# Kernel tuning notes

Measured on AMD Instinct MI355X. Metric: run time of the kernel, lower is better.

The kernel has to match this reference:

```python
import jax, jax.numpy as jnp
import numpy as np
from jax import lax

DIM = 384
NUM_HEADS = 8
KV_NUM_HEADS = 2
REP = NUM_HEADS // KV_NUM_HEADS  # 4
KV_DIM = DIM * 2 // REP          # 192
EPS_LN = 1e-5
EPS_NORM = 1e-12


def _layernorm_channel(x, w, b):
    # WithBias LayerNorm over channel dim of NCHW tensor (matches to_3d -> LN(c) -> to_4d)
    mu = jnp.mean(x, axis=1, keepdims=True)
    var = jnp.var(x, axis=1, keepdims=True)
    return (x - mu) / jnp.sqrt(var + EPS_LN) * w[None, :, None, None] + b[None, :, None, None]


def _conv1x1(x, w):
    # w: [out, in] ; x: [b, in, h, w]
    return jnp.einsum('oi,bihw->bohw', w, x)


def _dwconv3x3(x, w):
    # depthwise 3x3, padding=1; w: [C, 1, 3, 3]
    C = x.shape[1]
    return lax.conv_general_dilated(
        x, w, window_strides=(1, 1), padding=((1, 1), (1, 1)),
        feature_group_count=C,
        dimension_numbers=('NCHW', 'OIHW', 'NCHW'))


def _l2norm(x):
    n = jnp.linalg.norm(x, axis=-1, keepdims=True)
    return x / jnp.maximum(n, EPS_NORM)


def setup_inputs() -> dict:
    key = jax.random.key(0)
    ks = jax.random.split(key, 8)
    b, h, w = 8, 128, 128
    scale1 = 1.0 / np.sqrt(DIM)
    return {
        'q': jax.random.normal(ks[0], (b, DIM, h, w), dtype=jnp.float32),
        'k': jax.random.normal(ks[1], (b, DIM, h, w), dtype=jnp.float32),
        'w_q': jax.random.normal(ks[2], (DIM, DIM), dtype=jnp.float32) * scale1,
        'w_kv': jax.random.normal(ks[3], (KV_DIM, DIM), dtype=jnp.float32) * scale1,
        'w_q_dw': jax.random.normal(ks[4], (DIM, 1, 3, 3), dtype=jnp.float32) * (1.0 / 3.0),
        'w_kv_dw': jax.random.normal(ks[5], (KV_DIM, 1, 3, 3), dtype=jnp.float32) * (1.0 / 3.0),
        'w_out': jax.random.normal(ks[6], (DIM, DIM), dtype=jnp.float32) * scale1,
        'temperature': jnp.ones((NUM_HEADS, 1, 1), dtype=jnp.float32),
        'lnq_w': jnp.ones((DIM,), dtype=jnp.float32),
        'lnq_b': jnp.zeros((DIM,), dtype=jnp.float32),
        'lnk_w': jnp.ones((DIM,), dtype=jnp.float32),
        'lnk_b': jnp.zeros((DIM,), dtype=jnp.float32),
    }


def reference(q, k, w_q, w_kv, w_q_dw, w_kv_dw, w_out, temperature,
              lnq_w, lnq_b, lnk_w, lnk_b):
    b, c, h, w = q.shape
    hw = h * w
    qn = _layernorm_channel(q, lnq_w, lnq_b)
    kn = _layernorm_channel(k, lnk_w, lnk_b)
    qp = _dwconv3x3(_conv1x1(qn, w_q), w_q_dw)          # [b, dim, h, w]
    kv = _dwconv3x3(_conv1x1(kn, w_kv), w_kv_dw)        # [b, 2*dim/rep, h, w]
    kk, vv = jnp.split(kv, 2, axis=1)                   # each [b, dim/rep, h, w]
    # reshape to heads: channel-attention layout [b, head, c_head, hw]
    qh = qp.reshape(b, NUM_HEADS, DIM // NUM_HEADS, hw)
    kh = kk.reshape(b, KV_NUM_HEADS, DIM // NUM_HEADS, hw)
    vh = vv.reshape(b, KV_NUM_HEADS, DIM // NUM_HEADS, hw)
    # GQA repeat kv heads (repeat_interleave on head dim)
    kh = jnp.repeat(kh, REP, axis=1)
    vh = jnp.repeat(vh, REP, axis=1)
    qh = _l2norm(qh)
    kh = _l2norm(kh)
    attn = jnp.einsum('bhck,bhdk->bhcd', qh, kh) * temperature[None]
    attn = jax.nn.softmax(attn, axis=-1)
    out = jnp.einsum('bhcd,bhdk->bhck', attn, vh)       # [b, head, c_head, hw]
    out = out.reshape(b, DIM, h, w)
    return _conv1x1(out, w_out)
```

## Files before the change

kernel.cpp:

```cpp
#include <hip/hip_runtime.h>
#include <math.h>


typedef unsigned short u16;
typedef unsigned int u32;
typedef short s16x8 __attribute__((ext_vector_type(8)));
typedef float f32x4 __attribute__((ext_vector_type(4)));

#define HW 16384
#define NB 8
#define CDIM 384
#define KVC 192

__device__ __forceinline__ float b2f(u16 u) {
  return __uint_as_float(((u32)u) << 16);
}
__device__ __forceinline__ u16 f2b(float f) {
  u32 u = __float_as_uint(f);
  u += 0x7fffu + ((u >> 16) & 1u);
  return (u16)(u >> 16);
}
__device__ __forceinline__ u32 pack2(float a, float c) {
  return (u32)f2b(a) | ((u32)f2b(c) << 16);
}

__global__ void k0_prep(const float* __restrict__ wq, const float* __restrict__ wkv,
                        const float* __restrict__ wo,
                        const float* __restrict__ lnqw, const float* __restrict__ lnqb,
                        const float* __restrict__ lnkw, const float* __restrict__ lnkb,
                        u16* __restrict__ wqp, float* __restrict__ rwsQ, float* __restrict__ biasQ,
                        u16* __restrict__ wkvp, float* __restrict__ rwsKV, float* __restrict__ biasKV,
                        u16* __restrict__ wop) {
  int r = blockIdx.x * 256 + threadIdx.x;
  if (r < 384) {
    float rs = 0.f, bs = 0.f;
    for (int i = 0; i < 384; ++i) {
      float wp = wq[r * 384 + i] * lnqw[i];
      u16 h = f2b(wp);
      rs += b2f(h);
      bs += wq[r * 384 + i] * lnqb[i];
      wqp[r * 384 + i] = h;
    }
    rwsQ[r] = rs; biasQ[r] = bs;
  } else if (r < 768) {
    int o = r - 384;
    if (o < 192) {
      float rs = 0.f, bs = 0.f;
      for (int i = 0; i < 384; ++i) {
        float wp = wkv[o * 384 + i] * lnkw[i];
        u16 h = f2b(wp);
        rs += b2f(h);
        bs += wkv[o * 384 + i] * lnkb[i];
        wkvp[o * 384 + i] = h;
      }
      rwsKV[o] = rs; biasKV[o] = bs;
    } else {
      for (int i = 0; i < 384; ++i) wkvp[o * 384 + i] = 0;
      rwsKV[o] = 0.f; biasKV[o] = 0.f;
    }
  } else if (r < 1152) {
    int o = r - 768;
    for (int i = 0; i < 384; ++i) wop[o * 384 + i] = f2b(wo[o * 384 + i]);
  }
}

__global__ __launch_bounds__(512, 4) void gemm_qkv(const u16* __restrict__ Aq,
                                                   const u16* __restrict__ Akv,
                                                   const float* __restrict__ qsrc,
                                                   const float* __restrict__ ksrc,
                                                   const float* __restrict__ rwsQ,
                                                   const float* __restrict__ biasQ,
                                                   const float* __restrict__ rwsKV,
                                                   const float* __restrict__ biasKV,
                                                   u16* __restrict__ qp, u16* __restrict__ kvp) {
  __shared__ __align__(16) char smem[53760];
  u16*    tB   = (u16*)smem;
  float2* sred = (float2*)(smem + 49152);
  float*  muL  = (float*)(smem + 53248);
  float*  sdL  = (float*)(smem + 53504);
  u16*    chB16 = (u16*)smem;

  const int zz = blockIdx.z;
  const bool isQ = (zz < 8);
  const int b = zz & 7;
  const u16* A = isQ ? Aq : Akv;
  const float* Bf = isQ ? qsrc : ksrc;
  const float* rowsum = isQ ? rwsQ : rwsKV;
  const float* bias = isQ ? biasQ : biasKV;
  u16* outp = isQ ? qp : kvp;
  const int M = isQ ? 384 : 192;

  const int pt = ((blockIdx.x & 7) << 5) | (blockIdx.x >> 3);
  const int tid = threadIdx.x;
  const int w = tid >> 6, l = tid & 63;
  const int lr = l & 15, lg = l >> 4;

  f32x4 acc[3][4] = {};

  {
    const size_t fbase = (size_t)b * CDIM * HW + (size_t)pt * 64 + l;
    float v[48];
#pragma unroll
    for (int it = 0; it < 12; ++it)
#pragma unroll
      for (int j = 0; j < 4; ++j)
        v[it * 4 + j] = Bf[fbase + (size_t)(it * 32 + w * 4 + j) * HW];

    float s_ = 0.f, q_ = 0.f;
#pragma unroll
    for (int it = 0; it < 12; ++it) {
      float v0 = v[it * 4], v1 = v[it * 4 + 1], v2 = v[it * 4 + 2], v3 = v[it * 4 + 3];
      s_ += (v0 + v1) + (v2 + v3);
      q_ += (v0 * v0 + v1 * v1) + (v2 * v2 + v3 * v3);
      u32 lo = pack2(v0, v1), hi = pack2(v2, v3);
      int cidx = it * 4 + (w >> 1);
      int off = l * 384 + ((cidx ^ (l & 7)) << 3) + (w & 1) * 4;
      *(uint2*)&tB[off] = make_uint2(lo, hi);
    }
    sred[w * 64 + l] = make_float2(s_, q_);
  }
  __syncthreads();

  if (tid < 64) {
    float s = 0.f, q2 = 0.f;
#pragma unroll
    for (int g = 0; g < 8; ++g) { float2 t = sred[g * 64 + tid]; s += t.x; q2 += t.y; }
    float mn = s * (1.f / 384.f);
    float var = q2 * (1.f / 384.f) - mn * mn;
    muL[tid] = mn;
    sdL[tid] = rsqrtf(var + 1e-5f);
  }
  __syncthreads();

  s16x8 a[2][3], bb[2][4];
#pragma unroll
  for (int mf = 0; mf < 3; ++mf)
    a[0][mf] = *(const s16x8*)(A + (size_t)(w * 48 + mf * 16 + lr) * 384 + lg * 8);
#pragma unroll
  for (int nf = 0; nf < 4; ++nf) {
    int row = nf * 16 + lr;
    bb[0][nf] = *(const s16x8*)&tB[row * 384 + ((lg ^ (row & 7)) << 3)];
  }
#pragma unroll
  for (int ks = 0; ks < 12; ++ks) {
    const int cur = ks & 1, nxt = cur ^ 1;
    if (ks < 11) {
      const int ko = (ks + 1) * 32 + lg * 8;
      const int cidx = (ks + 1) * 4 + lg;
#pragma unroll
      for (int mf = 0; mf < 3; ++mf)
        a[nxt][mf] = *(const s16x8*)(A + (size_t)(w * 48 + mf * 16 + lr) * 384 + ko);
#pragma unroll
      for (int nf = 0; nf < 4; ++nf) {
        int row = nf * 16 + lr;
        bb[nxt][nf] = *(const s16x8*)&tB[row * 384 + ((cidx ^ (row & 7)) << 3)];
      }
    }
#pragma unroll
    for (int mf = 0; mf < 3; ++mf)
#pragma unroll
      for (int nf = 0; nf < 4; ++nf)
        acc[mf][nf] = __builtin_amdgcn_mfma_f32_16x16x32_bf16(a[cur][mf], bb[cur][nf], acc[mf][nf], 0, 0, 0);
  }

#pragma unroll
  for (int cc = 0; cc < 2; ++cc) {
    __syncthreads();
    if ((w >> 2) == cc) {
#pragma unroll
      for (int nf = 0; nf < 4; ++nf) {
        int prow = nf * 16 + lr;
        float m_ = muL[prow], s_ = sdL[prow];
#pragma unroll
        for (int mf = 0; mf < 3; ++mf)
#pragma unroll
          for (int r = 0; r < 4; ++r) {
            int orow = w * 48 + mf * 16 + lg * 4 + r;
            float v = s_ * (acc[mf][nf][r] - m_ * rowsum[orow]) + bias[orow];
            chB16[((w & 3) * 48 + mf * 16 + lg * 4 + r) * 72 + prow] = f2b(v);
          }
      }
    }
    __syncthreads();
    for (int i = tid; i < 192 * 8; i += 512) {
      int row = i >> 3, c8 = i & 7;
      int g = cc * 192 + row;
      if (g < M) {
        uint4 v = *(const uint4*)&chB16[row * 72 + c8 * 8];
        *(uint4*)(outp + ((size_t)(b * M + g)) * HW + pt * 64 + c8 * 8) = v;
      }
    }
  }
}

__global__ __launch_bounds__(256) void k4_dw(const u16* __restrict__ qp, const u16* __restrict__ kvp,
                                             const float* __restrict__ wqdw, const float* __restrict__ wkvdw,
                                             u16* __restrict__ qd, u16* __restrict__ kvd,
                                             float* __restrict__ rnq, float* __restrict__ rnk) {
  __shared__ u16 plane[16384];
  __shared__ float red[256];

  int c = blockIdx.x, b = blockIdx.y;
  int tid = threadIdx.x;
  const u16* in; u16* outb; const float* wp; int C;
  int isQ = (c < 384), cc = isQ ? c : c - 384;
  if (isQ) { in = qp; outb = qd; wp = wqdw + cc * 9; C = CDIM; }
  else     { in = kvp; outb = kvd; wp = wkvdw + cc * 9; C = KVC; }
  size_t base = ((size_t)(b * C + cc)) * HW;

  float w[9];
#pragma unroll
  for (int j = 0; j < 9; ++j) w[j] = wp[j];

  const uint4* gsrc = (const uint4*)(in + base);
  uint4* lplane = (uint4*)plane;
#pragma unroll
  for (int i = 0; i < 8; ++i) lplane[tid + i * 256] = gsrc[tid + i * 256];
  __syncthreads();

  uint4* gdst = (uint4*)(outb + base);
  float ns = 0.f;
#pragma unroll
  for (int it = 0; it < 8; ++it) {
    int idx = tid + it * 256;
    int y = idx >> 4, ox = idx & 15;
    int x0 = ox * 8;

    float r[3][10];
#pragma unroll
    for (int rr = 0; rr < 3; ++rr) {
      int yy = y + rr - 1;
      if ((unsigned)yy < 128u) {
        int rbase = yy * 128 + x0;
        r[rr][0] = (x0 > 0) ? b2f(plane[rbase - 1]) : 0.f;
        uint4 v = *(const uint4*)&plane[rbase];
        u32 ws[4] = {v.x, v.y, v.z, v.w};
#pragma unroll
        for (int j = 0; j < 4; ++j) {
          r[rr][1 + 2 * j] = b2f((u16)(ws[j] & 0xffff));
          r[rr][2 + 2 * j] = b2f((u16)(ws[j] >> 16));
        }
        r[rr][9] = (x0 < 120) ? b2f(plane[rbase + 8]) : 0.f;
      } else {
#pragma unroll
        for (int j = 0; j < 10; ++j) r[rr][j] = 0.f;
      }
    }

    u32 packed[4];
#pragma unroll
    for (int j = 0; j < 8; ++j) {
      float a = 0.f;
#pragma unroll
      for (int rr = 0; rr < 3; ++rr)
#pragma unroll
        for (int dx = 0; dx < 3; ++dx)
          a += w[rr * 3 + dx] * r[rr][j + dx];
      u16 h = f2b(a);
      float hv = b2f(h);
      ns += hv * hv;
      if (j & 1) packed[j >> 1] |= ((u32)h) << 16; else packed[j >> 1] = (u32)h;
    }
    gdst[idx] = make_uint4(packed[0], packed[1], packed[2], packed[3]);
  }

  red[tid] = ns;
  __syncthreads();
  for (int st = 128; st > 0; st >>= 1) {
    if (tid < st) red[tid] += red[tid + st];
    __syncthreads();
  }
  if (tid == 0) {
    float n = sqrtf(red[0]);
    float inv = 1.f / fmaxf(n, 1e-12f);
    if (isQ) rnq[b * 384 + cc] = inv;
    else if (cc < 96) rnk[b * 96 + cc] = inv;
  }
}

__global__ void k5b_vt(const u16* __restrict__ kvd, u16* __restrict__ vt) {
  int p = blockIdx.x * 256 + threadIdx.x;
  int b = blockIdx.y;
  size_t sb = ((size_t)(b * KVC + 96)) * HW + p;
  uint4* dv = (uint4*)vt + ((size_t)(b * HW + p)) * 12;
  for (int j8 = 0; j8 < 12; ++j8) {
    u32 w[4];
#pragma unroll
    for (int j = 0; j < 8; ++j) {
      u16 h = kvd[sb + (size_t)(j8 * 8 + j) * HW];
      if (j & 1) w[j >> 1] |= ((u32)h) << 16; else w[j >> 1] = (u32)h;
    }
    dv[j8] = make_uint4(w[0], w[1], w[2], w[3]);
  }
}

__global__ __launch_bounds__(256) void k6_qk(const u16* __restrict__ qd,
                                             const u16* __restrict__ kvd,
                                             float* __restrict__ spart) {
  int kc = blockIdx.x, h = blockIdx.y, b = blockIdx.z;
  int tid = threadIdx.x;
  int w = tid >> 6, l = tid & 63, lr = l & 15, lg = l >> 4;
  int g = h >> 2;
  int p0 = kc * 1024 + w * 256;

  f32x4 acc[3][3] = {};
  size_t qbase = ((size_t)(b * CDIM + h * 48 + lr)) * HW;
  size_t kbase = ((size_t)(b * KVC + g * 48 + lr)) * HW;

  for (int ks = 0; ks < 8; ++ks) {
    int pp = p0 + ks * 32 + lg * 8;
    s16x8 a[3], bb[3];
#pragma unroll
    for (int mi = 0; mi < 3; ++mi) a[mi] = *(const s16x8*)(qd + qbase + (size_t)mi * 16 * HW + pp);
#pragma unroll
    for (int ni = 0; ni < 3; ++ni) bb[ni] = *(const s16x8*)(kvd + kbase + (size_t)ni * 16 * HW + pp);
#pragma unroll
    for (int mi = 0; mi < 3; ++mi)
#pragma unroll
      for (int ni = 0; ni < 3; ++ni)
        acc[mi][ni] = __builtin_amdgcn_mfma_f32_16x16x32_bf16(a[mi], bb[ni], acc[mi][ni], 0, 0, 0);
  }

  size_t sb = ((size_t)((((b * 8 + h) * 16) + kc) * 4 + w)) * 2304;
#pragma unroll
  for (int mi = 0; mi < 3; ++mi)
#pragma unroll
    for (int ni = 0; ni < 3; ++ni)
#pragma unroll
      for (int r = 0; r < 4; ++r) {
        int c = mi * 16 + lg * 4 + r, d = ni * 16 + lr;
        spart[sb + c * 48 + d] = acc[mi][ni][r];
      }
}

__global__ void k7_sm(const float* __restrict__ spart, const float* __restrict__ temp,
                      const float* __restrict__ rnq, const float* __restrict__ rnk,
                      u16* __restrict__ ptil) {
  int h = blockIdx.x, b = blockIdx.y, tid = threadIdx.x;
  int g = h >> 2;
  __shared__ float S[2304];
  size_t base = ((size_t)((b * 8 + h) * 64)) * 2304;
  for (int e = tid; e < 2304; e += 64) {
    float s = 0.f;
    for (int j = 0; j < 64; ++j) s += spart[base + (size_t)j * 2304 + e];
    S[e] = s;
  }
  __syncthreads();
  if (tid < 48) {
    int c = tid;
    float sq = temp[h] * rnq[b * 384 + h * 48 + c];
    float mx = -1e30f;
    for (int d = 0; d < 48; ++d) {
      float v = S[c * 48 + d] * sq * rnk[b * 96 + g * 48 + d];
      mx = fmaxf(mx, v);
    }
    float sum = 0.f;
    for (int d = 0; d < 48; ++d) {
      float v = S[c * 48 + d] * sq * rnk[b * 96 + g * 48 + d];
      sum += __expf(v - mx);
    }
    float inv = 1.f / sum;
    u16* row = ptil + ((size_t)(b * 384 + h * 48 + c)) * 96;
    for (int dk = 0; dk < 96; ++dk) {
      int d = dk - g * 48;
      float pv = 0.f;
      if (d >= 0 && d < 48) {
        float v = S[c * 48 + d] * sq * rnk[b * 96 + g * 48 + d];
        pv = __expf(v - mx) * inv;
      }
      row[dk] = f2b(pv);
    }
  }
}

__global__ __launch_bounds__(512, 4) void k8_out(const u16* __restrict__ vt,
                                                 const u16* __restrict__ ptil,
                                                 const u16* __restrict__ wop,
                                                 float* __restrict__ out) {
  __shared__ __align__(16) char smem[62464];
  u16* tB = (u16*)smem;
  u16* tV = (u16*)(smem + 49152);
  float* chB32 = (float*)smem;

  const int b = blockIdx.z;
  const int pt = ((blockIdx.x & 7) << 5) | (blockIdx.x >> 3);
  const int tid = threadIdx.x;
  const int w = tid >> 6, l = tid & 63;
  const int lr = l & 15, lg = l >> 4;

  {
    int c0 = tid;
    int row = c0 / 12, cc = c0 % 12;
    uint4 v = *(const uint4*)(vt + ((size_t)(b * HW + pt * 64 + row)) * 96 + cc * 8);
    *(uint4*)&tV[row * 104 + cc * 8] = v;
    if (tid < 256) {
      int c1 = 512 + tid;
      int row1 = c1 / 12, cc1 = c1 % 12;
      uint4 v1 = *(const uint4*)(vt + ((size_t)(b * HW + pt * 64 + row1)) * 96 + cc1 * 8);
      *(uint4*)&tV[row1 * 104 + cc1 * 8] = v1;
    }
  }
  __syncthreads();

  {
    f32x4 accA[3][4] = {};
#pragma unroll
    for (int ks = 0; ks < 3; ++ks) {
      s16x8 a[3], bb[4];
#pragma unroll
      for (int mf = 0; mf < 3; ++mf)
        a[mf] = *(const s16x8*)(ptil + ((size_t)(b * 384 + w * 48 + mf * 16 + lr)) * 96 + ks * 32 + lg * 8);
#pragma unroll
      for (int nf = 0; nf < 4; ++nf)
        bb[nf] = *(const s16x8*)&tV[(nf * 16 + lr) * 104 + ks * 32 + lg * 8];
#pragma unroll
      for (int mf = 0; mf < 3; ++mf)
#pragma unroll
        for (int nf = 0; nf < 4; ++nf)
          accA[mf][nf] = __builtin_amdgcn_mfma_f32_16x16x32_bf16(a[mf], bb[nf], accA[mf][nf], 0, 0, 0);
    }
#pragma unroll
    for (int mf = 0; mf < 3; ++mf)
#pragma unroll
      for (int nf = 0; nf < 4; ++nf) {
        int prow = nf * 16 + lr;
        int cbase = w * 48 + mf * 16 + lg * 4;
        u32 lo = pack2(accA[mf][nf][0], accA[mf][nf][1]);
        u32 hi = pack2(accA[mf][nf][2], accA[mf][nf][3]);
        int chunk = (cbase >> 3) ^ (prow & 7);
        int off = prow * 384 + chunk * 8 + (cbase & 7);
        *(uint2*)&tB[off] = make_uint2(lo, hi);
      }
  }
  __syncthreads();

  f32x4 acc[3][4] = {};
  {
    s16x8 a[2][3], bb[2][4];
#pragma unroll
    for (int mf = 0; mf < 3; ++mf)
      a[0][mf] = *(const s16x8*)(wop + (size_t)(w * 48 + mf * 16 + lr) * 384 + lg * 8);
#pragma unroll
    for (int nf = 0; nf < 4; ++nf) {
      int row = nf * 16 + lr;
      bb[0][nf] = *(const s16x8*)&tB[row * 384 + ((lg ^ (row & 7)) << 3)];
    }
#pragma unroll
    for (int ks = 0; ks < 12; ++ks) {
      const int cur = ks & 1, nxt = cur ^ 1;
      if (ks < 11) {
        const int ko = (ks + 1) * 32 + lg * 8;
        const int cidx = (ks + 1) * 4 + lg;
#pragma unroll
        for (int mf = 0; mf < 3; ++mf)
          a[nxt][mf] = *(const s16x8*)(wop + (size_t)(w * 48 + mf * 16 + lr) * 384 + ko);
#pragma unroll
        for (int nf = 0; nf < 4; ++nf) {
          int row = nf * 16 + lr;
          bb[nxt][nf] = *(const s16x8*)&tB[row * 384 + ((cidx ^ (row & 7)) << 3)];
        }
      }
#pragma unroll
      for (int mf = 0; mf < 3; ++mf)
#pragma unroll
        for (int nf = 0; nf < 4; ++nf)
          acc[mf][nf] = __builtin_amdgcn_mfma_f32_16x16x32_bf16(a[cur][mf], bb[cur][nf], acc[mf][nf], 0, 0, 0);
    }
  }

#pragma unroll
  for (int cc = 0; cc < 2; ++cc) {
    __syncthreads();
    if ((w >> 2) == cc) {
#pragma unroll
      for (int nf = 0; nf < 4; ++nf) {
        int prow = nf * 16 + lr;
#pragma unroll
        for (int mf = 0; mf < 3; ++mf)
#pragma unroll
          for (int r = 0; r < 4; ++r) {
            int orow_l = (w & 3) * 48 + mf * 16 + lg * 4 + r;
            chB32[orow_l * 72 + prow] = acc[mf][nf][r];
          }
      }
    }
    __syncthreads();
    for (int i = tid; i < 192 * 16; i += 512) {
      int row = i >> 4, c4 = i & 15;
      uint4 v = *(const uint4*)&chB32[row * 72 + c4 * 4];
      *(uint4*)(out + ((size_t)(b * CDIM + cc * 192 + row)) * HW + pt * 64 + c4 * 4) = v;
    }
  }
}

extern "C" void kernel_launch(void* const* d_in, const int* in_sizes, int n_in,
                              void* d_out, int out_size, void* d_ws, size_t ws_size,
                              hipStream_t stream) {
  const float* q    = (const float*)d_in[0];
  const float* k    = (const float*)d_in[1];
  const float* w_q  = (const float*)d_in[2];
  const float* w_kv = (const float*)d_in[3];
  const float* w_qd = (const float*)d_in[4];
  const float* w_kd = (const float*)d_in[5];
  const float* w_o  = (const float*)d_in[6];
  const float* temp = (const float*)d_in[7];
  const float* lnqw = (const float*)d_in[8];
  const float* lnqb = (const float*)d_in[9];
  const float* lnkw = (const float*)d_in[10];
  const float* lnkb = (const float*)d_in[11];
  float* out = (float*)d_out;

  char* ws = (char*)d_ws;
  size_t off = 0;
  auto alloc = [&](size_t bytes) -> void* {
    void* p = ws + off;
    off += (bytes + 255) & ~(size_t)255;
    return p;
  };

  u16*   wqp   = (u16*)alloc(384 * 384 * 2);
  float* rwsQ  = (float*)alloc(384 * 4);
  float* biasQ = (float*)alloc(384 * 4);
  u16*   wkvp  = (u16*)alloc(384 * 384 * 2);
  float* rwsKV = (float*)alloc(384 * 4);
  float* biasKV= (float*)alloc(384 * 4);
  u16*   wop   = (u16*)alloc(384 * 384 * 2);
  u16*   qp    = (u16*)alloc((size_t)NB * CDIM * HW * 2);
  u16*   kvp   = (u16*)alloc((size_t)NB * KVC * HW * 2);
  u16*   qd    = (u16*)alloc((size_t)NB * CDIM * HW * 2);
  u16*   kvd   = (u16*)alloc((size_t)NB * KVC * HW * 2);
  u16*   vt    = (u16*)alloc((size_t)NB * HW * 96 * 2);
  float* spart = (float*)alloc((size_t)4096 * 2304 * 4);
  u16*   ptil  = (u16*)alloc((size_t)NB * CDIM * 96 * 2);
  float* rnq   = (float*)alloc((size_t)NB * 384 * 4);
  float* rnk   = (float*)alloc((size_t)NB * 96 * 4);

  k0_prep<<<5, 256, 0, stream>>>(w_q, w_kv, w_o, lnqw, lnqb, lnkw, lnkb,
                                 wqp, rwsQ, biasQ, wkvp, rwsKV, biasKV, wop);

  gemm_qkv<<<dim3(256, 1, 16), 512, 0, stream>>>(wqp, wkvp, q, k,
                                                 rwsQ, biasQ, rwsKV, biasKV, qp, kvp);

  k4_dw<<<dim3(576, NB), 256, 0, stream>>>(qp, kvp, w_qd, w_kd, qd, kvd, rnq, rnk);

  k5b_vt<<<dim3(64, NB), 256, 0, stream>>>(kvd, vt);

  k6_qk<<<dim3(16, 8, NB), 256, 0, stream>>>(qd, kvd, spart);
  k7_sm<<<dim3(8, NB), 64, 0, stream>>>(spart, temp, rnq, rnk, ptil);

  k8_out<<<dim3(256, 1, NB), 512, 0, stream>>>(vt, ptil, wop, out);
}
```

Before: 638.6 us.

## Stage QKV GEMM inputs via global_load_lds and split into two launches

The fused QKV projection GEMM now copies fp32 activations straight from global memory into LDS with global_load_lds instead of holding 48 values per thread in registers. The A fragment load is issued before the barrier so it overlaps the staging copy. The Q and KV projections become two separate launches of one kernel. LDS use grows to about 152KB, so launch bounds drop to 2 blocks per CU, and this occupancy loss may offset the reduced register pressure.

```diff
diff --git a/kernel.cpp b/kernel.cpp
--- a/kernel.cpp
+++ b/kernel.cpp
@@ -22,6 +22,11 @@
 }
 __device__ __forceinline__ u32 pack2(float a, float c) {
   return (u32)f2b(a) | ((u32)f2b(c) << 16);
+}
+__device__ __forceinline__ void gll4(const void* g, void* l) {
+  __builtin_amdgcn_global_load_lds(
+      (const __attribute__((address_space(1))) u32*)g,
+      (__attribute__((address_space(3))) u32*)l, 4, 0, 0);
 }
 
 __global__ void k0_prep(const float* __restrict__ wq, const float* __restrict__ wkv,
@@ -64,32 +69,20 @@
   }
 }
 
-__global__ __launch_bounds__(512, 4) void gemm_qkv(const u16* __restrict__ Aq,
-                                                   const u16* __restrict__ Akv,
-                                                   const float* __restrict__ qsrc,
-                                                   const float* __restrict__ ksrc,
-                                                   const float* __restrict__ rwsQ,
-                                                   const float* __restrict__ biasQ,
-                                                   const float* __restrict__ rwsKV,
-                                                   const float* __restrict__ biasKV,
-                                                   u16* __restrict__ qp, u16* __restrict__ kvp) {
-  __shared__ __align__(16) char smem[53760];
-  u16*    tB   = (u16*)smem;
-  float2* sred = (float2*)(smem + 49152);
-  float*  muL  = (float*)(smem + 53248);
-  float*  sdL  = (float*)(smem + 53504);
+__global__ __launch_bounds__(512, 2) void gemm_p(const u16* __restrict__ A,
+                                                 const float* __restrict__ Bf,
+                                                 const float* __restrict__ rowsum,
+                                                 const float* __restrict__ bias,
+                                                 u16* __restrict__ outp, int M) {
+  __shared__ __align__(16) char smem[152064];
+  float*  stg  = (float*)smem;
+  u16*    tile = (u16*)(smem + 98304);
+  float2* sred = (float2*)(smem + 147456);
+  float*  muL  = (float*)(smem + 151552);
+  float*  sdL  = (float*)(smem + 151808);
   u16*    chB16 = (u16*)smem;
 
-  const int zz = blockIdx.z;
-  const bool isQ = (zz < 8);
-  const int b = zz & 7;
-  const u16* A = isQ ? Aq : Akv;
-  const float* Bf = isQ ? qsrc : ksrc;
-  const float* rowsum = isQ ? rwsQ : rwsKV;
-  const float* bias = isQ ? biasQ : biasKV;
-  u16* outp = isQ ? qp : kvp;
-  const int M = isQ ? 384 : 192;
-
+  const int b = blockIdx.z;
   const int pt = ((blockIdx.x & 7) << 5) | (blockIdx.x >> 3);
   const int tid = threadIdx.x;
   const int w = tid >> 6, l = tid & 63;
@@ -98,24 +91,35 @@
   f32x4 acc[3][4] = {};
 
   {
-    const size_t fbase = (size_t)b * CDIM * HW + (size_t)pt * 64 + l;
-    float v[48];
-#pragma unroll
-    for (int it = 0; it < 12; ++it)
-#pragma unroll
-      for (int j = 0; j < 4; ++j)
-        v[it * 4 + j] = Bf[fbase + (size_t)(it * 32 + w * 4 + j) * HW];
-
+    const float* src = Bf + (size_t)b * CDIM * HW + (size_t)(w * 48) * HW
+                       + (size_t)pt * 64 + l;
+#pragma unroll
+    for (int i = 0; i < 48; ++i)
+      gll4(src + (size_t)i * HW, stg + (w * 48 + i) * 64);
+  }
+
+  s16x8 a[2][3], bb[2][4];
+#pragma unroll
+  for (int mf = 0; mf < 3; ++mf)
+    a[0][mf] = *(const s16x8*)(A + (size_t)(w * 48 + mf * 16 + lr) * 384 + lg * 8);
+
+  __syncthreads();
+
+  {
     float s_ = 0.f, q_ = 0.f;
 #pragma unroll
-    for (int it = 0; it < 12; ++it) {
-      float v0 = v[it * 4], v1 = v[it * 4 + 1], v2 = v[it * 4 + 2], v3 = v[it * 4 + 3];
+    for (int i = 0; i < 12; ++i) {
+      int c0 = w * 48 + i * 4;
+      float v0 = stg[(c0 + 0) * 64 + l];
+      float v1 = stg[(c0 + 1) * 64 + l];
+      float v2 = stg[(c0 + 2) * 64 + l];
+      float v3 = stg[(c0 + 3) * 64 + l];
       s_ += (v0 + v1) + (v2 + v3);
       q_ += (v0 * v0 + v1 * v1) + (v2 * v2 + v3 * v3);
       u32 lo = pack2(v0, v1), hi = pack2(v2, v3);
-      int cidx = it * 4 + (w >> 1);
-      int off = l * 384 + ((cidx ^ (l & 7)) << 3) + (w & 1) * 4;
-      *(uint2*)&tB[off] = make_uint2(lo, hi);
+      int cidx = c0 >> 3;
+      int off = l * 384 + ((cidx ^ (l & 7)) << 3) + (c0 & 7);
+      *(uint2*)&tile[off] = make_uint2(lo, hi);
     }
     sred[w * 64 + l] = make_float2(s_, q_);
   }
@@ -132,14 +136,10 @@
   }
   __syncthreads();
 
-  s16x8 a[2][3], bb[2][4];
-#pragma unroll
-  for (int mf = 0; mf < 3; ++mf)
-    a[0][mf] = *(const s16x8*)(A + (size_t)(w * 48 + mf * 16 + lr) * 384 + lg * 8);
 #pragma unroll
   for (int nf = 0; nf < 4; ++nf) {
     int row = nf * 16 + lr;
-    bb[0][nf] = *(const s16x8*)&tB[row * 384 + ((lg ^ (row & 7)) << 3)];
+    bb[0][nf] = *(const s16x8*)&tile[row * 384 + ((lg ^ (row & 7)) << 3)];
   }
 #pragma unroll
   for (int ks = 0; ks < 12; ++ks) {
@@ -153,7 +153,7 @@
 #pragma unroll
       for (int nf = 0; nf < 4; ++nf) {
         int row = nf * 16 + lr;
-        bb[nxt][nf] = *(const s16x8*)&tB[row * 384 + ((cidx ^ (row & 7)) << 3)];
+        bb[nxt][nf] = *(const s16x8*)&tile[row * 384 + ((cidx ^ (row & 7)) << 3)];
       }
     }
 #pragma unroll
@@ -538,8 +538,8 @@
   k0_prep<<<5, 256, 0, stream>>>(w_q, w_kv, w_o, lnqw, lnqb, lnkw, lnkb,
                                  wqp, rwsQ, biasQ, wkvp, rwsKV, biasKV, wop);
 
-  gemm_qkv<<<dim3(256, 1, 16), 512, 0, stream>>>(wqp, wkvp, q, k,
-                                                 rwsQ, biasQ, rwsKV, biasKV, qp, kvp);
+  gemm_p<<<dim3(256, 1, NB), 512, 0, stream>>>(wqp, q, rwsQ, biasQ, qp, 384);
+  gemm_p<<<dim3(256, 1, NB), 512, 0, stream>>>(wkvp, k, rwsKV, biasKV, kvp, 192);
 
   k4_dw<<<dim3(576, NB), 256, 0, stream>>>(qp, kvp, w_qd, w_kd, qd, kvd, rnq, rnk);
 
```

Result: slower. 658.2 us (+3.1%).
